# Kernel tuning notes

Measured on AMD Instinct MI355X. Metric: run time of the kernel, lower is better.

The kernel has to match this reference:

```python
import jax, jax.numpy as jnp
import numpy as np

H = 4
NEG_SLOPE = 0.2
N_P, N_A = 100000, 100000
E = 500000
L = 200000
F_IN, F_HID, F_OUT = 128, 128, 64


def setup_inputs() -> dict:
    key = jax.random.key(0)
    ks = jax.random.split(key, 32)
    s = 0.1  # weight init scale
    inp = {
        'x_paper': jax.random.normal(ks[0], (N_P, F_IN), jnp.float32),
        'x_author': jax.random.normal(ks[1], (N_A, F_IN), jnp.float32),
        'ei_pa': jax.random.randint(ks[2], (2, E), 0, N_P, jnp.int32),
        'ei_ap': jax.random.randint(ks[3], (2, E), 0, N_A, jnp.int32),
        'edge_label_index': jax.random.randint(ks[4], (2, L), 0, N_P, jnp.int32),
        # layer 1 params
        'p1W': s * jax.random.normal(ks[5], (F_IN, F_HID), jnp.float32),
        'p1b': jnp.zeros((F_HID,), jnp.float32),
        'a1W': s * jax.random.normal(ks[6], (F_IN, F_HID), jnp.float32),
        'a1b': jnp.zeros((F_HID,), jnp.float32),
        's1pa': s * jax.random.normal(ks[7], (H, F_HID // H), jnp.float32),
        'd1pa': s * jax.random.normal(ks[8], (H, F_HID // H), jnp.float32),
        's1ap': s * jax.random.normal(ks[9], (H, F_HID // H), jnp.float32),
        'd1ap': s * jax.random.normal(ks[10], (H, F_HID // H), jnp.float32),
        'k1W': s * jax.random.normal(ks[11], (F_HID, F_HID), jnp.float32),
        'k1b': jnp.zeros((F_HID,), jnp.float32),
        'q1': s * jax.random.normal(ks[12], (F_HID,), jnp.float32),
        # layer 2 params
        'p2W': s * jax.random.normal(ks[13], (F_HID, F_OUT), jnp.float32),
        'p2b': jnp.zeros((F_OUT,), jnp.float32),
        'a2W': s * jax.random.normal(ks[14], (F_HID, F_OUT), jnp.float32),
        'a2b': jnp.zeros((F_OUT,), jnp.float32),
        's2pa': s * jax.random.normal(ks[15], (H, F_OUT // H), jnp.float32),
        'd2pa': s * jax.random.normal(ks[16], (H, F_OUT // H), jnp.float32),
        's2ap': s * jax.random.normal(ks[17], (H, F_OUT // H), jnp.float32),
        'd2ap': s * jax.random.normal(ks[18], (H, F_OUT // H), jnp.float32),
        'k2W': s * jax.random.normal(ks[19], (F_OUT, F_OUT), jnp.float32),
        'k2b': jnp.zeros((F_OUT,), jnp.float32),
        'q2': s * jax.random.normal(ks[20], (F_OUT,), jnp.float32),
    }
    return inp


def _edge_attn(h_src, h_dst, src, dst, a_src, a_dst, num_dst):
    # h_*: [N, H, D]; a_*: [H, D]. Per-edge node-level GAT-style attention.
    alpha = (jnp.einsum('nhd,hd->nh', h_src, a_src)[src]
             + jnp.einsum('nhd,hd->nh', h_dst, a_dst)[dst])  # [E, H]
    alpha = jnp.where(alpha >= 0, alpha, NEG_SLOPE * alpha)  # leaky_relu
    amax = jax.ops.segment_max(alpha, dst, num_segments=num_dst)
    amax = jnp.where(jnp.isfinite(amax), amax, 0.0)
    ex = jnp.exp(alpha - amax[dst])
    denom = jax.ops.segment_sum(ex, dst, num_segments=num_dst)
    w = ex / (denom[dst] + 1e-16)
    out = jax.ops.segment_sum(h_src[src] * w[:, :, None], dst, num_segments=num_dst)
    return jax.nn.relu(out).reshape(num_dst, -1)  # [N_dst, H*D]


def _group(xs, q, kW, kb):
    # Semantic-level attention over metapaths (PyG HANConv `group`).
    out = jnp.stack(xs)  # [M, N, F]
    score = (q * jnp.tanh(out @ kW + kb).mean(axis=1)).sum(-1)  # [M]
    attn = jax.nn.softmax(score)
    return (attn[:, None, None] * out).sum(0)


def _han_layer(x_p, x_a, ei_pa, ei_ap, pW, pb, aW, ab, s_pa, d_pa, s_ap, d_ap, kW, kb, q):
    D = pW.shape[1] // H
    h_p = (x_p @ pW + pb).reshape(-1, H, D)
    h_a = (x_a @ aW + ab).reshape(-1, H, D)
    out_a = _edge_attn(h_p, h_a, ei_pa[0], ei_pa[1], s_pa, d_pa, h_a.shape[0])
    out_p = _edge_attn(h_a, h_p, ei_ap[0], ei_ap[1], s_ap, d_ap, h_p.shape[0])
    z_p = _group([out_p], q, kW, kb)
    z_a = _group([out_a], q, kW, kb)
    return z_p, z_a


def reference(x_paper, x_author, ei_pa, ei_ap, edge_label_index,
              p1W, p1b, a1W, a1b, s1pa, d1pa, s1ap, d1ap, k1W, k1b, q1,
              p2W, p2b, a2W, a2b, s2pa, d2pa, s2ap, d2ap, k2W, k2b, q2):
    z_p, z_a = _han_layer(x_paper, x_author, ei_pa, ei_ap,
                          p1W, p1b, a1W, a1b, s1pa, d1pa, s1ap, d1ap, k1W, k1b, q1)
    z_p, z_a = _han_layer(z_p, z_a, ei_pa, ei_ap,
                          p2W, p2b, a2W, a2b, s2pa, d2pa, s2ap, d2ap, k2W, k2b, q2)
    src = z_p[edge_label_index[0]]
    dst = z_a[edge_label_index[1]]
    return (src * dst).sum(axis=-1)  # [L]
```

## Files before the change

### kernel.cpp

```cpp
#include <hip/hip_runtime.h>


#define HEADS 4

typedef _Float16 f16x8 __attribute__((ext_vector_type(8)));
typedef _Float16 f16x4 __attribute__((ext_vector_type(4)));
typedef float    f32x4 __attribute__((ext_vector_type(4)));

__device__ __forceinline__ float leaky02(float a) {
    return a >= 0.f ? a : 0.2f * a;
}

__device__ __forceinline__ void prep_one(const float* W, _Float16* Wf, int M, int o) {
    const int v = o & 7, lane = (o >> 3) & 63, rest = o >> 9;
    const int jl = rest & 3, t = (rest >> 2) & 3, grp = rest >> 4;
    const int k = t * 32 + (lane >> 4) * 8 + v;
    const int n = (grp * 4 + jl) * 16 + (lane & 15);
    Wf[o] = (_Float16)W[k * M + n];
}

__global__ __launch_bounds__(256) void prep_w4(
    const float* __restrict__ W1, _Float16* __restrict__ Wf1,
    const float* __restrict__ W2, _Float16* __restrict__ Wf2,
    const float* __restrict__ W3, _Float16* __restrict__ Wf3,
    const float* __restrict__ W4, _Float16* __restrict__ Wf4) {
    int o = blockIdx.x * 256 + threadIdx.x;
    if (o < 16384)       prep_one(W1, Wf1, 128, o);
    else if (o < 32768)  prep_one(W2, Wf2, 128, o - 16384);
    else if (o < 40960)  prep_one(W3, Wf3, 64, o - 32768);
    else if (o < 49152)  prep_one(W4, Wf4, 64, o - 40960);
}

template<int M, bool AHALF>
__global__ __launch_bounds__(256) void gemm_mfma_dual(
    const void* __restrict__ XA, const _Float16* __restrict__ WfA,
    const float* __restrict__ bA, _Float16* __restrict__ outA,
    const float* __restrict__ svA, const float* __restrict__ dvA,
    float* __restrict__ asA, float* __restrict__ adA,
    const void* __restrict__ XB, const _Float16* __restrict__ WfB,
    const float* __restrict__ bB, _Float16* __restrict__ outB,
    const float* __restrict__ svB, const float* __restrict__ dvB,
    float* __restrict__ asB, float* __restrict__ adB,
    int N, int nbs) {
    constexpr int NSPLIT = (M == 128) ? 2 : 1;
    constexpr int JT  = 4;
    constexpr int D   = M / HEADS;
    constexpr int HPB = 64 / D;
    constexpr int HL  = 4 / HPB;
    constexpr int SA  = 136;
    constexpr int WFH = JT * 4 * 64 * 8;
    __shared__ _Float16 lds_a[64 * SA];
    __shared__ _Float16 lds_w[WFH];

    const bool second = blockIdx.x >= (unsigned)nbs;
    const void* __restrict__ X      = second ? XB : XA;
    const _Float16* __restrict__ Wf = second ? WfB : WfA;
    const float* __restrict__ b     = second ? bB : bA;
    _Float16* __restrict__ out      = second ? outB : outA;
    const float* __restrict__ sv    = second ? svB : svA;
    const float* __restrict__ dv    = second ? dvB : dvA;
    float* __restrict__ asb         = second ? asB : asA;
    float* __restrict__ adb         = second ? adB : adA;
    const int b0    = second ? blockIdx.x - nbs : blockIdx.x;
    const int brow  = b0 / NSPLIT;
    const int split = b0 % NSPLIT;
    const int row0  = brow * 64;
    const int colb  = split * 64;

    const int wave = threadIdx.x >> 6;
    const int lane = threadIdx.x & 63;
    const int m    = lane & 15;
    const int quad = lane >> 4;

    {
        const _Float16* wsrc = Wf + split * WFH;
        const int base = threadIdx.x * 8;
        #pragma unroll
        for (int it = 0; it < WFH / 2048; ++it) {
            f16x8 v = *(const f16x8*)(wsrc + it * 2048 + base);
            *(f16x8*)(lds_w + it * 2048 + base) = v;
        }
    }
    if (AHALF) {
        #pragma unroll
        for (int it = 0; it < 4; ++it) {
            const int r = it * 16 + (threadIdx.x >> 4);
            const int k = (threadIdx.x & 15) * 8;
            int gr = row0 + r; if (gr >= N) gr = N - 1;
            f16x8 v = *(const f16x8*)((const _Float16*)X + (size_t)gr * 128 + k);
            *(f16x8*)(lds_a + r * SA + k) = v;
        }
    } else {
        #pragma unroll
        for (int it = 0; it < 8; ++it) {
            const int r = it * 8 + (threadIdx.x >> 5);
            const int k = (threadIdx.x & 31) * 4;
            int gr = row0 + r; if (gr >= N) gr = N - 1;
            float4 v = *(const float4*)((const float*)X + (size_t)gr * 128 + k);
            f16x4 h = {(_Float16)v.x, (_Float16)v.y, (_Float16)v.z, (_Float16)v.w};
            *(f16x4*)(lds_a + r * SA + k) = h;
        }
    }
    __syncthreads();

    f32x4 acc[JT];
    #pragma unroll
    for (int j = 0; j < JT; ++j) acc[j] = (f32x4){0.f, 0.f, 0.f, 0.f};

    const int ab = (wave * 16 + m) * SA;
    #pragma unroll
    for (int t = 0; t < 4; ++t) {
        f16x8 a = *(const f16x8*)(lds_a + ab + t * 32 + quad * 8);
        #pragma unroll
        for (int j = 0; j < JT; ++j) {
            f16x8 bf = *(const f16x8*)(lds_w + ((t * JT + j) * 64 + lane) * 8);
            acc[j] = __builtin_amdgcn_mfma_f32_16x16x32_f16(a, bf, acc[j], 0, 0, 0);
        }
    }

    #pragma unroll
    for (int j = 0; j < JT; ++j) {
        const float bias = b[colb + j * 16 + m];
        #pragma unroll
        for (int r = 0; r < 4; ++r)
            lds_a[(wave * 16 + quad * 4 + r) * SA + j * 16 + m] =
                (_Float16)(acc[j][r] + bias);
    }

    {
        const int r = lane >> 2;
        const int q = lane & 3;
        float ps = 0.f, pd = 0.f;
        #pragma unroll
        for (int j = 0; j < 4; ++j) {
            f16x4 v4 = *(const f16x4*)(&lds_a[(wave * 16 + r) * SA + q * 16 + 4 * j]);
            float4 s4 = *(const float4*)(sv + colb + q * 16 + 4 * j);
            float4 d4 = *(const float4*)(dv + colb + q * 16 + 4 * j);
            const float v0 = (float)v4[0], v1 = (float)v4[1],
                        v2 = (float)v4[2], v3 = (float)v4[3];
            ps += v0 * s4.x + v1 * s4.y + v2 * s4.z + v3 * s4.w;
            pd += v0 * d4.x + v1 * d4.y + v2 * d4.z + v3 * d4.w;
        }
        if (HL == 2) { ps += __shfl_xor(ps, 1); pd += __shfl_xor(pd, 1); }
        const int grow = row0 + wave * 16 + r;
        if (grow < N && (q & (HL - 1)) == 0) {
            const int hh = split * HPB + q / HL;
            asb[(size_t)grow * HEADS + hh] = ps;
            adb[(size_t)grow * HEADS + hh] = pd;
        }
    }

    {
        const int lr = lane & 15;
        const int rq = lane >> 4;
        #pragma unroll
        for (int i = 0; i < 4; ++i) {
            const int lrow = i * 4 + rq;
            const int grow = row0 + wave * 16 + lrow;
            if (grow < N) {
                f16x4 v = *(const f16x4*)(&lds_a[(wave * 16 + lrow) * SA + lr * 4]);
                *(f16x4*)(out + (size_t)grow * M + colb + lr * 4) = v;
            }
        }
    }
}

__global__ __launch_bounds__(256) void hist_dual(
    const int* __restrict__ dst_pa, const int* __restrict__ dst_ap,
    int* __restrict__ counts, int N, int E) {
    const int eg = blockIdx.x * 256 + threadIdx.x;
    if (eg >= 2 * E) return;
    const int idx = (eg < E) ? dst_pa[eg] : (N + dst_ap[eg - E]);
    atomicAdd(counts + idx, 1);
}

__global__ __launch_bounds__(256) void scan_blk(
    const int* __restrict__ in, int* __restrict__ out,
    int* __restrict__ bsum, int N) {
    __shared__ int sh[256];
    const int base = blockIdx.x * 1024 + threadIdx.x * 4;
    int v[4]; int s = 0;
    #pragma unroll
    for (int j = 0; j < 4; ++j) { v[j] = (base + j < N) ? in[base + j] : 0; s += v[j]; }
    sh[threadIdx.x] = s;
    __syncthreads();
    for (int off = 1; off < 256; off <<= 1) {
        int t = (threadIdx.x >= off) ? sh[threadIdx.x - off] : 0;
        __syncthreads();
        sh[threadIdx.x] += t;
        __syncthreads();
    }
    int run = sh[threadIdx.x] - s;
    #pragma unroll
    for (int j = 0; j < 4; ++j) {
        if (base + j < N) out[base + j] = run;
        run += v[j];
    }
    if (threadIdx.x == 255) bsum[blockIdx.x] = sh[255];
}

__global__ __launch_bounds__(256) void scan_sums(int* __restrict__ bsum, int nb) {
    __shared__ int sh[256];
    int v = (threadIdx.x < nb) ? bsum[threadIdx.x] : 0;
    sh[threadIdx.x] = v;
    __syncthreads();
    for (int off = 1; off < 256; off <<= 1) {
        int t = (threadIdx.x >= off) ? sh[threadIdx.x - off] : 0;
        __syncthreads();
        sh[threadIdx.x] += t;
        __syncthreads();
    }
    if (threadIdx.x < nb) bsum[threadIdx.x] = sh[threadIdx.x] - v;
}

__global__ __launch_bounds__(256) void scan_add(
    int* __restrict__ out, const int* __restrict__ bsum, int N) {
    const int base = blockIdx.x * 1024 + threadIdx.x * 4;
    const int add = bsum[blockIdx.x];
    #pragma unroll
    for (int j = 0; j < 4; ++j)
        if (base + j < N) out[base + j] += add;
}

__global__ __launch_bounds__(256) void scatter_dual(
    const int* __restrict__ src_pa, const int* __restrict__ dst_pa,
    const int* __restrict__ src_ap, const int* __restrict__ dst_ap,
    const int* __restrict__ offsets, int* __restrict__ cursor,
    int* __restrict__ perm, int N, int E) {
    const int eg = blockIdx.x * 256 + threadIdx.x;
    if (eg >= 2 * E) return;
    int idx, val;
    if (eg < E) { idx = dst_pa[eg];         val = src_pa[eg]; }
    else        { idx = N + dst_ap[eg - E]; val = src_ap[eg - E]; }
    const int pos = offsets[idx] + atomicAdd(cursor + idx, 1);
    perm[pos] = val;
}

__global__ __launch_bounds__(256) void deg_hist(
    const int* __restrict__ cnt, int* __restrict__ bhist, int n2) {
    __shared__ int lh[128];
    if (threadIdx.x < 128) lh[threadIdx.x] = 0;
    __syncthreads();
    const int N = n2 >> 1;
    for (int i = blockIdx.x * 256 + threadIdx.x; i < n2; i += gridDim.x * 256) {
        int c = cnt[i]; if (c > 63) c = 63;
        atomicAdd(&lh[(i >= N ? 64 : 0) + c], 1);
    }
    __syncthreads();
    if (threadIdx.x < 128) atomicAdd(&bhist[threadIdx.x], lh[threadIdx.x]);
}

__global__ __launch_bounds__(256) void deg_scatter(
    const int* __restrict__ cnt, int* __restrict__ bcur,
    int* __restrict__ order, int n2) {
    __shared__ int lh[128];
    __shared__ int lbase[128];
    if (threadIdx.x < 128) lh[threadIdx.x] = 0;
    __syncthreads();
    const int N = n2 >> 1;
    const int i = blockIdx.x * 256 + threadIdx.x;
    int key = 0, lpos = 0;
    if (i < n2) {
        int c = cnt[i]; if (c > 63) c = 63;
        key = (i >= N ? 64 : 0) + c;
        lpos = atomicAdd(&lh[key], 1);
    }
    __syncthreads();
    if (threadIdx.x < 128 && lh[threadIdx.x] > 0)
        lbase[threadIdx.x] = atomicAdd(&bcur[threadIdx.x], lh[threadIdx.x]);
    __syncthreads();
    if (i < n2) order[lbase[key] + lpos] = i;
}

__global__ __launch_bounds__(256) void agg_proj_dual(
    const int* __restrict__ order,
    const int* __restrict__ perm, const int* __restrict__ offsets,
    const int* __restrict__ counts,
    const float* __restrict__ as1_0, const float* __restrict__ ad1_0,
    const _Float16* __restrict__ h1_0,
    const _Float16* __restrict__ Wf_0, const float* __restrict__ bb_0,
    _Float16* __restrict__ h2_0,
    const float* __restrict__ sv_0, const float* __restrict__ dv_0,
    float* __restrict__ as2_0, float* __restrict__ ad2_0,
    const float* __restrict__ as1_1, const float* __restrict__ ad1_1,
    const _Float16* __restrict__ h1_1,
    const _Float16* __restrict__ Wf_1, const float* __restrict__ bb_1,
    _Float16* __restrict__ h2_1,
    const float* __restrict__ sv_1, const float* __restrict__ dv_1,
    float* __restrict__ as2_1, float* __restrict__ ad2_1,
    int N, int GB) {
    constexpr int SAF = 136;
    constexpr int SH  = 72;
    __shared__ _Float16 ldsW[8192];
    __shared__ _Float16 ldsA[16 * SAF];
    __shared__ _Float16 ldsH[16 * SH];

    const bool d1 = blockIdx.x >= (unsigned)GB;
    const float*    __restrict__ as1 = d1 ? as1_1 : as1_0;
    const float*    __restrict__ ad1 = d1 ? ad1_1 : ad1_0;
    const _Float16* __restrict__ h1  = d1 ? h1_1 : h1_0;
    const _Float16* __restrict__ Wf  = d1 ? Wf_1 : Wf_0;
    const float*    __restrict__ bb  = d1 ? bb_1 : bb_0;
    _Float16*       __restrict__ h2  = d1 ? h2_1 : h2_0;
    const float*    __restrict__ sv  = d1 ? sv_1 : sv_0;
    const float*    __restrict__ dv  = d1 ? dv_1 : dv_0;
    float*          __restrict__ as2 = d1 ? as2_1 : as2_0;
    float*          __restrict__ ad2 = d1 ? ad2_1 : ad2_0;
    const int b0    = d1 ? blockIdx.x - GB : blockIdx.x;
    const int dbase = d1 ? N : 0;

    const int tid  = threadIdx.x;
    const int wave = tid >> 6;
    const int lane = tid & 63;
    const int nk   = tid >> 4;
    const int fl   = tid & 15;
    const int f0   = fl * 8;
    const int hh   = fl >> 2;
    const int m    = lane & 15;
    const int quad = lane >> 4;

    {
        const int base = tid * 8;
        #pragma unroll
        for (int it = 0; it < 4; ++it) {
            f16x8 v = *(const f16x8*)(Wf + it * 2048 + base);
            *(f16x8*)(ldsW + it * 2048 + base) = v;
        }
    }

    const int nG = (N + 15) >> 4;
    for (int g = b0; g < nG; g += GB) {
        f16x8 rowv;
        #pragma unroll
        for (int j = 0; j < 8; ++j) rowv[j] = (_Float16)0.f;
        const int idx = g * 16 + nk;
        if (idx < N) {
            const int node_g = order[dbase + (N - 1 - idx)];
            const int node   = node_g - dbase;
            const int start  = offsets[node_g];
            const int cnt    = counts[node_g];
            const float ad   = ad1[(size_t)node * HEADS + hh];
            float den = 0.f;
            float acc[8];
            #pragma unroll
            for (int j = 0; j < 8; ++j) acc[j] = 0.f;
            const int last = cnt - 1;
            for (int i = 0; i < cnt; i += 4) {
                const int i1 = (i + 1 < cnt) ? i + 1 : last;
                const int i2 = (i + 2 < cnt) ? i + 2 : last;
                const int i3 = (i + 3 < cnt) ? i + 3 : last;
                const int s0 = perm[start + i];
                const int s1 = perm[start + i1];
                const int s2 = perm[start + i2];
                const int s3 = perm[start + i3];
                const float a0 = as1[(size_t)s0 * HEADS + hh];
                const float a1 = as1[(size_t)s1 * HEADS + hh];
                const float a2 = as1[(size_t)s2 * HEADS + hh];
                const float a3 = as1[(size_t)s3 * HEADS + hh];
                f16x8 h0 = *(const f16x8*)(h1 + (size_t)s0 * 128 + f0);
                f16x8 hb = *(const f16x8*)(h1 + (size_t)s1 * 128 + f0);
                f16x8 hc = *(const f16x8*)(h1 + (size_t)s2 * 128 + f0);
                f16x8 hd = *(const f16x8*)(h1 + (size_t)s3 * 128 + f0);
                const float e0 = __expf(leaky02(a0 + ad));
                float e1 = __expf(leaky02(a1 + ad));
                float e2 = __expf(leaky02(a2 + ad));
                float e3 = __expf(leaky02(a3 + ad));
                if (i + 1 >= cnt) e1 = 0.f;
                if (i + 2 >= cnt) e2 = 0.f;
                if (i + 3 >= cnt) e3 = 0.f;
                den += (e0 + e1) + (e2 + e3);
                #pragma unroll
                for (int j = 0; j < 8; ++j)
                    acc[j] += e0 * (float)h0[j] + e1 * (float)hb[j]
                            + e2 * (float)hc[j] + e3 * (float)hd[j];
            }
            const float inv = 1.f / (den + 1e-16f);
            #pragma unroll
            for (int j = 0; j < 8; ++j)
                rowv[j] = (_Float16)fmaxf(acc[j] * inv, 0.f);
        }
        *(f16x8*)(ldsA + nk * SAF + f0) = rowv;
        __syncthreads();

        f32x4 c = (f32x4){0.f, 0.f, 0.f, 0.f};
        const int ab = m * SAF;
        #pragma unroll
        for (int t = 0; t < 4; ++t) {
            f16x8 a  = *(const f16x8*)(ldsA + ab + t * 32 + quad * 8);
            f16x8 bf = *(const f16x8*)(ldsW + ((t * 4 + wave) * 64 + lane) * 8);
            c = __builtin_amdgcn_mfma_f32_16x16x32_f16(a, bf, c, 0, 0, 0);
        }
        const float bias = bb[wave * 16 + m];
        #pragma unroll
        for (int r = 0; r < 4; ++r)
            ldsH[(quad * 4 + r) * SH + wave * 16 + m] = (_Float16)(c[r] + bias);
        __syncthreads();

        if (wave == 0) {
            const int r = lane >> 2;
            const int q = lane & 3;
            const int aidx = g * 16 + r;
            if (aidx < N) {
                const int anode = order[dbase + (N - 1 - aidx)] - dbase;
                float ps = 0.f, pd = 0.f;
                #pragma unroll
                for (int jj = 0; jj < 4; ++jj) {
                    f16x4 v4 = *(const f16x4*)(&ldsH[r * SH + q * 16 + 4 * jj]);
                    float4 s4 = *(const float4*)(sv + q * 16 + 4 * jj);
                    float4 d4 = *(const float4*)(dv + q * 16 + 4 * jj);
                    const float v0 = (float)v4[0], v1 = (float)v4[1],
                                v2 = (float)v4[2], v3 = (float)v4[3];
                    ps += v0 * s4.x + v1 * s4.y + v2 * s4.z + v3 * s4.w;
                    pd += v0 * d4.x + v1 * d4.y + v2 * d4.z + v3 * d4.w;
                }
                as2[(size_t)anode * HEADS + q] = ps;
                ad2[(size_t)anode * HEADS + q] = pd;
            }
        }
        {
            const int lr  = lane & 15;
            const int rq  = lane >> 4;
            const int row = wave * 4 + rq;
            const int sidx = g * 16 + row;
            if (sidx < N) {
                const int snode = order[dbase + (N - 1 - sidx)] - dbase;
                f16x4 v = *(const f16x4*)(&ldsH[row * SH + lr * 4]);
                *(f16x4*)(h2 + (size_t)snode * 64 + lr * 4) = v;
            }
        }
    }
}

template<int F, int D>
__global__ __launch_bounds__(256) void csr_attn_agg_dual(
    const int* __restrict__ order,
    const int* __restrict__ perm, const int* __restrict__ offsets,
    const int* __restrict__ counts,
    const float* __restrict__ asrcP, const float* __restrict__ adstP,
    const _Float16* __restrict__ hP, _Float16* __restrict__ outA,
    const float* __restrict__ asrcA, const float* __restrict__ adstA,
    const _Float16* __restrict__ hA, _Float16* __restrict__ outP,
    int N) {
    constexpr int LPN = F / 8;
    const int gid  = blockIdx.x * 256 + threadIdx.x;
    const int slotF = gid / LPN;
    const int lane  = gid % LPN;
    if (slotF >= 2 * N) return;
    const int slot = 2 * N - 1 - slotF;
    const int node_g = order[slot];
    const bool second = node_g >= N;
    const int node = second ? node_g - N : node_g;
    const float* __restrict__ asrc    = second ? asrcA : asrcP;
    const float* __restrict__ adst    = second ? adstA : adstP;
    const _Float16* __restrict__ hsrc = second ? hA : hP;
    _Float16* __restrict__ out        = second ? outP : outA;

    const int start = offsets[node_g];
    const int cnt   = counts[node_g];
    const int f0 = lane * 8;
    const int h  = f0 / D;
    const float ad = adst[(size_t)node * HEADS + h];

    float den = 0.f;
    float acc[8];
    #pragma unroll
    for (int j = 0; j < 8; ++j) acc[j] = 0.f;
    const int last = cnt - 1;
    for (int i = 0; i < cnt; i += 4) {
        const int i1 = (i + 1 < cnt) ? i + 1 : last;
        const int i2 = (i + 2 < cnt) ? i + 2 : last;
        const int i3 = (i + 3 < cnt) ? i + 3 : last;
        const int s0 = perm[start + i];
        const int s1 = perm[start + i1];
        const int s2 = perm[start + i2];
        const int s3 = perm[start + i3];
        const float a0 = asrc[(size_t)s0 * HEADS + h];
        const float a1 = asrc[(size_t)s1 * HEADS + h];
        const float a2 = asrc[(size_t)s2 * HEADS + h];
        const float a3 = asrc[(size_t)s3 * HEADS + h];
        f16x8 h0 = *(const f16x8*)(hsrc + (size_t)s0 * F + f0);
        f16x8 h1 = *(const f16x8*)(hsrc + (size_t)s1 * F + f0);
        f16x8 h2 = *(const f16x8*)(hsrc + (size_t)s2 * F + f0);
        f16x8 h3 = *(const f16x8*)(hsrc + (size_t)s3 * F + f0);
        const float e0 = __expf(leaky02(a0 + ad));
        float e1 = __expf(leaky02(a1 + ad));
        float e2 = __expf(leaky02(a2 + ad));
        float e3 = __expf(leaky02(a3 + ad));
        if (i + 1 >= cnt) e1 = 0.f;
        if (i + 2 >= cnt) e2 = 0.f;
        if (i + 3 >= cnt) e3 = 0.f;
        den += (e0 + e1) + (e2 + e3);
        #pragma unroll
        for (int j = 0; j < 8; ++j)
            acc[j] += e0 * (float)h0[j] + e1 * (float)h1[j]
                    + e2 * (float)h2[j] + e3 * (float)h3[j];
    }
    const float inv = 1.f / (den + 1e-16f);
    f16x8 o;
    #pragma unroll
    for (int j = 0; j < 8; ++j)
        o[j] = (_Float16)fmaxf(acc[j] * inv, 0.f);
    *(f16x8*)(out + (size_t)node * F + f0) = o;
}

__global__ __launch_bounds__(256) void edge_dot(
    const int* __restrict__ eli, const _Float16* __restrict__ zp,
    const _Float16* __restrict__ za, float* __restrict__ out, int L) {
    constexpr int LPE = 8;
    const int gid  = blockIdx.x * blockDim.x + threadIdx.x;
    const int e    = gid / LPE;
    const int lane = gid % LPE;
    if (e >= L) return;
    const int p = eli[e], a = eli[(size_t)L + e];
    f16x8 pv = *(const f16x8*)(zp + (size_t)p * 64 + lane * 8);
    f16x8 av = *(const f16x8*)(za + (size_t)a * 64 + lane * 8);
    float s = 0.f;
    #pragma unroll
    for (int j = 0; j < 8; ++j) s += (float)pv[j] * (float)av[j];
    #pragma unroll
    for (int off = 4; off > 0; off >>= 1) s += __shfl_xor(s, off);
    if (lane == 0) out[e] = s;
}

static inline int cdiv(long long a, long long b) { return (int)((a + b - 1) / b); }

extern "C" void kernel_launch(void* const* d_in, const int* in_sizes, int n_in,
                              void* d_out, int out_size, void* d_ws, size_t ws_size,
                              hipStream_t stream) {
    const float* x_p  = (const float*)d_in[0];
    const float* x_a  = (const float*)d_in[1];
    const int* ei_pa  = (const int*)d_in[2];
    const int* ei_ap  = (const int*)d_in[3];
    const int* eli    = (const int*)d_in[4];
    const float* p1W = (const float*)d_in[5];
    const float* p1b = (const float*)d_in[6];
    const float* a1W = (const float*)d_in[7];
    const float* a1b = (const float*)d_in[8];
    const float* s1pa = (const float*)d_in[9];
    const float* d1pa = (const float*)d_in[10];
    const float* s1ap = (const float*)d_in[11];
    const float* d1ap = (const float*)d_in[12];
    const float* p2W = (const float*)d_in[16];
    const float* p2b = (const float*)d_in[17];
    const float* a2W = (const float*)d_in[18];
    const float* a2b = (const float*)d_in[19];
    const float* s2pa = (const float*)d_in[20];
    const float* d2pa = (const float*)d_in[21];
    const float* s2ap = (const float*)d_in[22];
    const float* d2ap = (const float*)d_in[23];

    const int NP = in_sizes[0] / 128;
    const int E  = in_sizes[2] / 2;
    const int L  = in_sizes[4] / 2;
    const int N  = NP;

    char* ws = (char*)d_ws;
    size_t off = 0;
    auto alloc = [&](size_t bytes) -> char* {
        char* p = ws + off;
        off += (bytes + 255) & ~(size_t)255;
        return p;
    };
    _Float16* h_p1   = (_Float16*)alloc((size_t)N * 128 * 2);
    _Float16* h_a1   = (_Float16*)alloc((size_t)N * 128 * 2);
    _Float16* h_p2   = (_Float16*)alloc((size_t)N * 64 * 2);
    _Float16* h_a2   = (_Float16*)alloc((size_t)N * 64 * 2);
    _Float16* out_p2 = (_Float16*)alloc((size_t)N * 64 * 2);
    _Float16* out_a2 = (_Float16*)alloc((size_t)N * 64 * 2);
    float* asrc_pa = (float*)alloc((size_t)N * HEADS * 4);
    float* adst_pa = (float*)alloc((size_t)N * HEADS * 4);
    float* asrc_ap = (float*)alloc((size_t)N * HEADS * 4);
    float* adst_ap = (float*)alloc((size_t)N * HEADS * 4);
    float* as2_pa  = (float*)alloc((size_t)N * HEADS * 4);
    float* ad2_pa  = (float*)alloc((size_t)N * HEADS * 4);
    float* as2_ap  = (float*)alloc((size_t)N * HEADS * 4);
    float* ad2_ap  = (float*)alloc((size_t)N * HEADS * 4);
    _Float16* Wf1p = (_Float16*)alloc(16384 * 2);
    _Float16* Wf1a = (_Float16*)alloc(16384 * 2);
    _Float16* Wf2p = (_Float16*)alloc(8192 * 2);
    _Float16* Wf2a = (_Float16*)alloc(8192 * 2);
    int* cnt2    = (int*)alloc((size_t)2 * N * 4);
    int* cursor2 = (int*)alloc((size_t)2 * N * 4);
    int* bhist   = (int*)alloc(512);
    int* off2    = (int*)alloc((size_t)2 * N * 4);
    int* perm2   = (int*)alloc((size_t)2 * E * 4);
    int* order2  = (int*)alloc((size_t)2 * N * 4);
    int* bsum    = (int*)alloc(256 * 4);

    const int* src_pa = ei_pa;
    const int* dst_pa = ei_pa + E;
    const int* src_ap = ei_ap;
    const int* dst_ap = ei_ap + E;

    const int N2 = 2 * N;
    const int nbScan = cdiv(N2, 1024);

    prep_w4<<<cdiv(49152, 256), 256, 0, stream>>>(p1W, Wf1p, a1W, Wf1a, p2W, Wf2p, a2W, Wf2a);
    hipMemsetAsync(cnt2, 0, ((size_t)4 * N + 128) * 4, stream);
    hist_dual<<<cdiv((long long)2 * E, 256), 256, 0, stream>>>(dst_pa, dst_ap, cnt2, N, E);
    scan_blk<<<nbScan, 256, 0, stream>>>(cnt2, off2, bsum, N2);
    scan_sums<<<1, 256, 0, stream>>>(bsum, nbScan);
    scan_add<<<nbScan, 256, 0, stream>>>(off2, bsum, N2);
    scatter_dual<<<cdiv((long long)2 * E, 256), 256, 0, stream>>>(
        src_pa, dst_pa, src_ap, dst_ap, off2, cursor2, perm2, N, E);
    deg_hist<<<256, 256, 0, stream>>>(cnt2, bhist, N2);
    scan_sums<<<1, 256, 0, stream>>>(bhist, 128);
    deg_scatter<<<cdiv(N2, 256), 256, 0, stream>>>(cnt2, bhist, order2, N2);

    const int nbs1 = cdiv(N, 64) * 2;

    gemm_mfma_dual<128, false><<<2 * nbs1, 256, 0, stream>>>(
        x_p, Wf1p, p1b, h_p1, s1pa, d1ap, asrc_pa, adst_ap,
        x_a, Wf1a, a1b, h_a1, s1ap, d1pa, asrc_ap, adst_pa, N, nbs1);

    const int nG = cdiv(N, 16);
    const int GB = cdiv(nG, 10);
    agg_proj_dual<<<2 * GB, 256, 0, stream>>>(
        order2, perm2, off2, cnt2,
        asrc_pa, adst_pa, h_p1, Wf2a, a2b, h_a2, s2ap, d2pa, as2_ap, ad2_pa,
        asrc_ap, adst_ap, h_a1, Wf2p, p2b, h_p2, s2pa, d2ap, as2_pa, ad2_ap,
        N, GB);

    csr_attn_agg_dual<64, 16><<<cdiv((long long)N2 * 8, 256), 256, 0, stream>>>(
        order2, perm2, off2, cnt2,
        as2_pa, ad2_pa, h_p2, out_a2,
        as2_ap, ad2_ap, h_a2, out_p2, N);

    edge_dot<<<cdiv((long long)L * 8, 256), 256, 0, stream>>>(
        eli, out_p2, out_a2, (float*)d_out, L);
}
```

Measured before the change: 416.0 us.

## Fuse CSR scan and degree-bucket sort kernels; fix agg grid size

Folds the degree histogram into the block scan kernel, scans both block sums and the degree histogram in one two-block launch, and merges the scan-add pass with the degree-bucket scatter. This cuts the preprocessing chain from six small launches to three and drops one extra pass over the counts array. The agg_proj_dual grid is also pinned to a fixed 768 blocks per side instead of being derived from N. That relies on the kernel looping over its work (not shown), and a fixed grid may fit the GPU better or worse than the old size.

```diff
diff --git a/kernel.cpp b/kernel.cpp
--- a/kernel.cpp
+++ b/kernel.cpp
@@ -176,12 +176,24 @@
 
 __global__ __launch_bounds__(256) void scan_blk(
     const int* __restrict__ in, int* __restrict__ out,
-    int* __restrict__ bsum, int N) {
+    int* __restrict__ bsum, int* __restrict__ bhist, int N2) {
     __shared__ int sh[256];
+    __shared__ int lh[128];
+    if (threadIdx.x < 128) lh[threadIdx.x] = 0;
+    __syncthreads();
+    const int N = N2 >> 1;
     const int base = blockIdx.x * 1024 + threadIdx.x * 4;
     int v[4]; int s = 0;
     #pragma unroll
-    for (int j = 0; j < 4; ++j) { v[j] = (base + j < N) ? in[base + j] : 0; s += v[j]; }
+    for (int j = 0; j < 4; ++j) {
+        const int i = base + j;
+        v[j] = (i < N2) ? in[i] : 0;
+        s += v[j];
+        if (i < N2) {
+            int c = v[j] > 63 ? 63 : v[j];
+            atomicAdd(&lh[(i >= N ? 64 : 0) + c], 1);
+        }
+    }
     sh[threadIdx.x] = s;
     __syncthreads();
     for (int off = 1; off < 256; off <<= 1) {
@@ -193,15 +205,20 @@
     int run = sh[threadIdx.x] - s;
     #pragma unroll
     for (int j = 0; j < 4; ++j) {
-        if (base + j < N) out[base + j] = run;
+        if (base + j < N2) out[base + j] = run;
         run += v[j];
     }
     if (threadIdx.x == 255) bsum[blockIdx.x] = sh[255];
-}
-
-__global__ __launch_bounds__(256) void scan_sums(int* __restrict__ bsum, int nb) {
+    if (threadIdx.x < 128 && lh[threadIdx.x] > 0)
+        atomicAdd(&bhist[threadIdx.x], lh[threadIdx.x]);
+}
+
+__global__ __launch_bounds__(256) void scan_sums2(
+    int* __restrict__ bsum, int nb, int* __restrict__ bhist) {
     __shared__ int sh[256];
-    int v = (threadIdx.x < nb) ? bsum[threadIdx.x] : 0;
+    int* buf   = (blockIdx.x == 0) ? bsum : bhist;
+    const int n = (blockIdx.x == 0) ? nb : 128;
+    int v = (threadIdx.x < n) ? buf[threadIdx.x] : 0;
     sh[threadIdx.x] = v;
     __syncthreads();
     for (int off = 1; off < 256; off <<= 1) {
@@ -210,16 +227,40 @@
         sh[threadIdx.x] += t;
         __syncthreads();
     }
-    if (threadIdx.x < nb) bsum[threadIdx.x] = sh[threadIdx.x] - v;
-}
-
-__global__ __launch_bounds__(256) void scan_add(
-    int* __restrict__ out, const int* __restrict__ bsum, int N) {
+    if (threadIdx.x < n) buf[threadIdx.x] = sh[threadIdx.x] - v;
+}
+
+__global__ __launch_bounds__(256) void finalize_degscatter(
+    int* __restrict__ off2, const int* __restrict__ bsum,
+    const int* __restrict__ cnt, int* __restrict__ bcur,
+    int* __restrict__ order, int n2) {
+    __shared__ int lh[128];
+    __shared__ int lbase[128];
+    if (threadIdx.x < 128) lh[threadIdx.x] = 0;
+    __syncthreads();
+    const int N = n2 >> 1;
     const int base = blockIdx.x * 1024 + threadIdx.x * 4;
     const int add = bsum[blockIdx.x];
-    #pragma unroll
-    for (int j = 0; j < 4; ++j)
-        if (base + j < N) out[base + j] += add;
+    int key[4], lpos[4];
+    #pragma unroll
+    for (int j = 0; j < 4; ++j) {
+        const int i = base + j;
+        if (i < n2) {
+            off2[i] += add;
+            int c = cnt[i]; if (c > 63) c = 63;
+            key[j] = (i >= N ? 64 : 0) + c;
+            lpos[j] = atomicAdd(&lh[key[j]], 1);
+        }
+    }
+    __syncthreads();
+    if (threadIdx.x < 128 && lh[threadIdx.x] > 0)
+        lbase[threadIdx.x] = atomicAdd(&bcur[threadIdx.x], lh[threadIdx.x]);
+    __syncthreads();
+    #pragma unroll
+    for (int j = 0; j < 4; ++j) {
+        const int i = base + j;
+        if (i < n2) order[lbase[key[j]] + lpos[j]] = i;
+    }
 }
 
 __global__ __launch_bounds__(256) void scatter_dual(
@@ -234,42 +275,6 @@
     else        { idx = N + dst_ap[eg - E]; val = src_ap[eg - E]; }
     const int pos = offsets[idx] + atomicAdd(cursor + idx, 1);
     perm[pos] = val;
-}
-
-__global__ __launch_bounds__(256) void deg_hist(
-    const int* __restrict__ cnt, int* __restrict__ bhist, int n2) {
-    __shared__ int lh[128];
-    if (threadIdx.x < 128) lh[threadIdx.x] = 0;
-    __syncthreads();
-    const int N = n2 >> 1;
-    for (int i = blockIdx.x * 256 + threadIdx.x; i < n2; i += gridDim.x * 256) {
-        int c = cnt[i]; if (c > 63) c = 63;
-        atomicAdd(&lh[(i >= N ? 64 : 0) + c], 1);
-    }
-    __syncthreads();
-    if (threadIdx.x < 128) atomicAdd(&bhist[threadIdx.x], lh[threadIdx.x]);
-}
-
-__global__ __launch_bounds__(256) void deg_scatter(
-    const int* __restrict__ cnt, int* __restrict__ bcur,
-    int* __restrict__ order, int n2) {
-    __shared__ int lh[128];
-    __shared__ int lbase[128];
-    if (threadIdx.x < 128) lh[threadIdx.x] = 0;
-    __syncthreads();
-    const int N = n2 >> 1;
-    const int i = blockIdx.x * 256 + threadIdx.x;
-    int key = 0, lpos = 0;
-    if (i < n2) {
-        int c = cnt[i]; if (c > 63) c = 63;
-        key = (i >= N ? 64 : 0) + c;
-        lpos = atomicAdd(&lh[key], 1);
-    }
-    __syncthreads();
-    if (threadIdx.x < 128 && lh[threadIdx.x] > 0)
-        lbase[threadIdx.x] = atomicAdd(&bcur[threadIdx.x], lh[threadIdx.x]);
-    __syncthreads();
-    if (i < n2) order[lbase[key] + lpos] = i;
 }
 
 __global__ __launch_bounds__(256) void agg_proj_dual(
@@ -598,14 +603,11 @@
     prep_w4<<<cdiv(49152, 256), 256, 0, stream>>>(p1W, Wf1p, a1W, Wf1a, p2W, Wf2p, a2W, Wf2a);
     hipMemsetAsync(cnt2, 0, ((size_t)4 * N + 128) * 4, stream);
     hist_dual<<<cdiv((long long)2 * E, 256), 256, 0, stream>>>(dst_pa, dst_ap, cnt2, N, E);
-    scan_blk<<<nbScan, 256, 0, stream>>>(cnt2, off2, bsum, N2);
-    scan_sums<<<1, 256, 0, stream>>>(bsum, nbScan);
-    scan_add<<<nbScan, 256, 0, stream>>>(off2, bsum, N2);
+    scan_blk<<<nbScan, 256, 0, stream>>>(cnt2, off2, bsum, bhist, N2);
+    scan_sums2<<<2, 256, 0, stream>>>(bsum, nbScan, bhist);
+    finalize_degscatter<<<nbScan, 256, 0, stream>>>(off2, bsum, cnt2, bhist, order2, N2);
     scatter_dual<<<cdiv((long long)2 * E, 256), 256, 0, stream>>>(
         src_pa, dst_pa, src_ap, dst_ap, off2, cursor2, perm2, N, E);
-    deg_hist<<<256, 256, 0, stream>>>(cnt2, bhist, N2);
-    scan_sums<<<1, 256, 0, stream>>>(bhist, 128);
-    deg_scatter<<<cdiv(N2, 256), 256, 0, stream>>>(cnt2, bhist, order2, N2);
 
     const int nbs1 = cdiv(N, 64) * 2;
 
@@ -613,8 +615,7 @@
         x_p, Wf1p, p1b, h_p1, s1pa, d1ap, asrc_pa, adst_ap,
         x_a, Wf1a, a1b, h_a1, s1ap, d1pa, asrc_ap, adst_pa, N, nbs1);
 
-    const int nG = cdiv(N, 16);
-    const int GB = cdiv(nG, 10);
+    const int GB = 768;
     agg_proj_dual<<<2 * GB, 256, 0, stream>>>(
         order2, perm2, off2, cnt2,
         asrc_pa, adst_pa, h_p1, Wf2a, a2b, h_a2, s2ap, d2pa, as2_ap, ad2_pa,
```

Measured after the change: 419.8 us. About the same (+0.9%).
